# Optimization experiments

Measured on AMD Instinct MI355X. Metric: run time of the kernel, lower is better.

Reference implementation:

```python
import jax, jax.numpy as jnp
import numpy as np

B, S, HID = 16, 1, 2048
H, D = 32, 64
KV = 4096
SCALE = D ** -0.5


def setup_inputs() -> dict:
    key = jax.random.key(0)
    ks = jax.random.split(key, 5)
    x = jax.random.normal(ks[0], (B, S, HID), dtype=jnp.float32)
    bias = jax.random.normal(ks[1], (B, H, S, KV), dtype=jnp.float32)
    past_kv = jax.random.normal(ks[2], (2, B, H, KV, D), dtype=jnp.float32)
    # fused QKV projection weight: [3*H*D, hidden], no bias
    w_qkv = jax.random.normal(ks[3], (3 * H * D, HID), dtype=jnp.float32) * (HID ** -0.5)
    # output projection: [hidden, H*D]
    w_o = jax.random.normal(ks[4], (HID, H * D), dtype=jnp.float32) * (HID ** -0.5)
    return {"x": x, "bias": bias, "past_kv": past_kv, "w_qkv": w_qkv, "w_o": w_o}


def reference(x, bias, past_kv, w_qkv, w_o):
    # fused QKV projection: [B, S, 3*H*D]
    qkv = jnp.einsum('bsh,oh->bso', x, w_qkv)
    # -> [3, B, H, S, D]  (proj, heads interleaved as (proj heads head_dim))
    qkv = qkv.reshape(B, S, 3, H, D).transpose(2, 0, 3, 1, 4)
    q, k_new, v_new = qkv[0], qkv[1], qkv[2]
    # KV cache: keep first KV-1 entries, append current step's k/v as the last slot
    past_k = past_kv[0, :, :, : KV - 1]  # [B, H, KV-1, D]
    past_v = past_kv[1, :, :, : KV - 1]
    k = jnp.concatenate([past_k, k_new], axis=-2)  # [B, H, KV, D]
    v = jnp.concatenate([past_v, v_new], axis=-2)
    # SDPA with additive relative-position bias
    scores = jnp.einsum('bhqd,bhkd->bhqk', q, k) * SCALE + bias
    probs = jax.nn.softmax(scores, axis=-1)
    a = jnp.einsum('bhqk,bhkd->bhqd', probs, v)  # [B, H, S, D]
    a = a.transpose(0, 2, 1, 3).reshape(B, S, H * D)
    return jnp.einsum('bsf,of->bso', a, w_o)
```

## Files before the change

kernel.cpp:

```cpp
#include <hip/hip_runtime.h>
#include <math.h>

#define Bc     16
#define HIDc   2048
#define Hc     32
#define Dc     64
#define KVc    4096
#define QKVO   6144
#define SCALEc 0.125f
#define CHUNKS 4
#define CHUNK  1024

typedef float f4v __attribute__((ext_vector_type(4)));

__global__ __launch_bounds__(256) void qkv_kernel(const float* __restrict__ x,
                                                  const float* __restrict__ w,
                                                  float* __restrict__ qkv) {
    __shared__ float4 xs[512];
    int blk = blockIdx.x;
    int b   = blk & 15;
    int og  = blk >> 4;
    int t = threadIdx.x, lane = t & 63, wid = t >> 6;
    const float4* xr = reinterpret_cast<const float4*>(x + (size_t)b * HIDc);
    xs[t]       = xr[t];
    xs[t + 256] = xr[t + 256];
    __syncthreads();
    int o0 = og * 64 + wid * 16;
#pragma unroll 2
    for (int i = 0; i < 16; ++i) {
        int o = o0 + i;
        const float4* wr = reinterpret_cast<const float4*>(w + (size_t)o * HIDc);
        float acc = 0.f;
#pragma unroll
        for (int j = 0; j < 8; ++j) {
            float4 a = xs[lane + 64 * j];
            float4 c = wr[lane + 64 * j];
            acc += a.x * c.x + a.y * c.y + a.z * c.z + a.w * c.w;
        }
#pragma unroll
        for (int off = 32; off >= 1; off >>= 1) acc += __shfl_xor(acc, off);
        if (lane == 0) qkv[(size_t)b * QKVO + o] = acc;
    }
}

__global__ __launch_bounds__(256, 4) void attn_chunk_kernel(const float* __restrict__ qkv,
                                                            const float* __restrict__ bias,
                                                            const float* __restrict__ past_kv,
                                                            float* __restrict__ part_o,
                                                            float* __restrict__ part_s) {
    __shared__ float bs[CHUNK];
    __shared__ float accs[16][65];
    __shared__ float ps[16];

    int blk = blockIdx.x;
    int c   = blk & (CHUNKS - 1);
    int bh  = blk >> 2;
    int h   = bh & 31;
    int b   = bh >> 5;
    int t    = threadIdx.x;
    int lane = t & 63;
    int wid  = t >> 6;
    int sg   = lane >> 4;
    int cg   = lane & 15;
    int row0 = c * CHUNK;

    reinterpret_cast<float4*>(bs)[t] =
        reinterpret_cast<const float4*>(bias + (size_t)bh * KVc + row0)[t];

    const float* qp = qkv + (size_t)b * QKVO + h * Dc;
    float4 q4 = reinterpret_cast<const float4*>(qp)[cg];

    const size_t kvstride = (size_t)KVc * Dc;
    const float* pastK = past_kv + (size_t)bh * kvstride + (size_t)row0 * Dc;
    const float* pastV = past_kv + (size_t)(Bc * Hc) * kvstride + (size_t)bh * kvstride
                         + (size_t)row0 * Dc;

    __syncthreads();

    int rbase = wid * 4 + sg;
    float s = 0.f;
    float4 acc = {0.f, 0.f, 0.f, 0.f};

    f4v kA[4], vA[4], kB[4], vB[4];

    auto LOAD = [&](int ot, f4v (&k4)[4], f4v (&v4)[4]) {
        int it = ot * 4;
#pragma unroll
        for (int u = 0; u < 4; ++u) {
            int rl = (it + u) * 16 + rbase;
            k4[u] = __builtin_nontemporal_load(
                        reinterpret_cast<const f4v*>(pastK + (size_t)rl * Dc) + cg);
        }
#pragma unroll
        for (int u = 0; u < 4; ++u) {
            int rl = (it + u) * 16 + rbase;
            v4[u] = __builtin_nontemporal_load(
                        reinterpret_cast<const f4v*>(pastV + (size_t)rl * Dc) + cg);
        }
    };
    auto COMPUTE = [&](int ot, f4v (&k4)[4], f4v (&v4)[4]) {
        int it = ot * 4;
        float es = 0.f;
        float4 va = {0.f, 0.f, 0.f, 0.f};
#pragma unroll
        for (int u = 0; u < 4; ++u) {
            int rl = (it + u) * 16 + rbase;
            float pp = q4.x * k4[u].x + q4.y * k4[u].y + q4.z * k4[u].z + q4.w * k4[u].w;
            pp += __shfl_xor(pp, 1);
            pp += __shfl_xor(pp, 2);
            pp += __shfl_xor(pp, 4);
            pp += __shfl_xor(pp, 8);
            float e = __expf(fmaf(pp, SCALEc, bs[rl]));
            es += e;
            va.x = fmaf(e, v4[u].x, va.x);
            va.y = fmaf(e, v4[u].y, va.y);
            va.z = fmaf(e, v4[u].z, va.z);
            va.w = fmaf(e, v4[u].w, va.w);
        }
        s += es;
        acc.x += va.x;
        acc.y += va.y;
        acc.z += va.z;
        acc.w += va.w;
    };

    int nclean = (c == CHUNKS - 1) ? 15 : 16;
    LOAD(0, kA, vA);
    int ot = 0;
    while (true) {
        if (ot + 1 < nclean) LOAD(ot + 1, kB, vB);
        COMPUTE(ot, kA, vA);
        if (++ot >= nclean) break;
        if (ot + 1 < nclean) LOAD(ot + 1, kA, vA);
        COMPUTE(ot, kB, vB);
        if (++ot >= nclean) break;
    }

    if (c == CHUNKS - 1) {
        const float* knew = qkv + (size_t)b * QKVO + HIDc + h * Dc;
        const float* vnew = qkv + (size_t)b * QKVO + 2 * HIDc + h * Dc;
        int it = 60;
        float4 k4[4], v4[4];
#pragma unroll
        for (int u = 0; u < 4; ++u) {
            int rl = (it + u) * 16 + rbase;
            const float* kr = (rl == CHUNK - 1) ? knew : (pastK + (size_t)rl * Dc);
            k4[u] = reinterpret_cast<const float4*>(kr)[cg];
        }
#pragma unroll
        for (int u = 0; u < 4; ++u) {
            int rl = (it + u) * 16 + rbase;
            const float* vr = (rl == CHUNK - 1) ? vnew : (pastV + (size_t)rl * Dc);
            v4[u] = reinterpret_cast<const float4*>(vr)[cg];
        }
#pragma unroll
        for (int u = 0; u < 4; ++u) {
            int rl = (it + u) * 16 + rbase;
            float pp = q4.x * k4[u].x + q4.y * k4[u].y + q4.z * k4[u].z + q4.w * k4[u].w;
            pp += __shfl_xor(pp, 1);
            pp += __shfl_xor(pp, 2);
            pp += __shfl_xor(pp, 4);
            pp += __shfl_xor(pp, 8);
            float e = __expf(fmaf(pp, SCALEc, bs[rl]));
            s += e;
            acc.x = fmaf(e, v4[u].x, acc.x);
            acc.y = fmaf(e, v4[u].y, acc.y);
            acc.z = fmaf(e, v4[u].z, acc.z);
            acc.w = fmaf(e, v4[u].w, acc.w);
        }
    }

    int sgid = wid * 4 + sg;
    if (cg == 0) ps[sgid] = s;
    accs[sgid][cg * 4 + 0] = acc.x;
    accs[sgid][cg * 4 + 1] = acc.y;
    accs[sgid][cg * 4 + 2] = acc.z;
    accs[sgid][cg * 4 + 3] = acc.w;
    __syncthreads();
    if (t < 64) {
        float S = 0.f, o = 0.f;
#pragma unroll
        for (int i = 0; i < 16; ++i) {
            S += ps[i];
            o += accs[i][t];
        }
        part_o[((size_t)bh * CHUNKS + c) * Dc + t] = o;
        if (t == 0) part_s[(size_t)bh * CHUNKS + c] = S;
    }
}

__global__ __launch_bounds__(64) void attn_combine_kernel(const float* __restrict__ part_o,
                                                          const float* __restrict__ part_s,
                                                          float* __restrict__ attn_out) {
    int bh = blockIdx.x;
    int d  = threadIdx.x;
    float S = 0.f, o = 0.f;
#pragma unroll
    for (int c = 0; c < CHUNKS; ++c) {
        S += part_s[(size_t)bh * CHUNKS + c];
        o += part_o[((size_t)bh * CHUNKS + c) * Dc + d];
    }
    attn_out[(size_t)bh * Dc + d] = o / S;
}

__global__ __launch_bounds__(256) void outproj_kernel(const float* __restrict__ attn,
                                                      const float* __restrict__ w_o,
                                                      float* __restrict__ out) {
    __shared__ float4 as[512];
    int blk = blockIdx.x;
    int b   = blk & 15;
    int fg  = blk >> 4;
    int t = threadIdx.x, lane = t & 63, wid = t >> 6;
    const float4* ar = reinterpret_cast<const float4*>(attn + (size_t)b * HIDc);
    as[t]       = ar[t];
    as[t + 256] = ar[t + 256];
    __syncthreads();
    int f0 = fg * 64 + wid * 16;
#pragma unroll 2
    for (int i = 0; i < 16; ++i) {
        int f = f0 + i;
        const float4* wr = reinterpret_cast<const float4*>(w_o + (size_t)f * HIDc);
        float acc = 0.f;
#pragma unroll
        for (int j = 0; j < 8; ++j) {
            float4 a = as[lane + 64 * j];
            float4 c = wr[lane + 64 * j];
            acc += a.x * c.x + a.y * c.y + a.z * c.z + a.w * c.w;
        }
#pragma unroll
        for (int off = 32; off >= 1; off >>= 1) acc += __shfl_xor(acc, off);
        if (lane == 0) out[(size_t)b * HIDc + f] = acc;
    }
}

extern "C" void kernel_launch(void* const* d_in, const int* in_sizes, int n_in,
                              void* d_out, int out_size, void* d_ws, size_t ws_size,
                              hipStream_t stream) {
    const float* x       = (const float*)d_in[0];
    const float* bias    = (const float*)d_in[1];
    const float* past_kv = (const float*)d_in[2];
    const float* w_qkv   = (const float*)d_in[3];
    const float* w_o     = (const float*)d_in[4];
    float* out = (float*)d_out;

    float* qkv    = (float*)d_ws;
    float* attn   = qkv + (size_t)Bc * QKVO;
    float* part_o = attn + (size_t)Bc * HIDc;
    float* part_s = part_o + (size_t)Bc * Hc * CHUNKS * Dc;

    qkv_kernel<<<dim3(Bc * (QKVO / 64)), dim3(256), 0, stream>>>(x, w_qkv, qkv);
    attn_chunk_kernel<<<dim3(Bc * Hc * CHUNKS), dim3(256), 0, stream>>>(qkv, bias, past_kv, part_o, part_s);
    attn_combine_kernel<<<dim3(Bc * Hc), dim3(64), 0, stream>>>(part_o, part_s, attn);
    outproj_kernel<<<dim3(Bc * (HIDc / 64)), dim3(256), 0, stream>>>(attn, w_o, out);
}
```

Measured before the change: 245.5 us.

## Batch eight rows per block in GEMVs and fuse combine into out-projection

The QKV and output projection kernels now process eight batch rows per block, so each weight row is loaded once per eight batch rows instead of once per row. The split-KV combine step is folded into the output projection's shared-memory staging, removing a separate kernel launch and the intermediate attention buffer. The cost is a 64KB shared-memory footprint per block, fewer blocks, and more accumulator registers, which may reduce occupancy.

```diff
diff --git a/kernel.cpp b/kernel.cpp
--- a/kernel.cpp
+++ b/kernel.cpp
@@ -13,33 +13,42 @@
 
 typedef float f4v __attribute__((ext_vector_type(4)));
 
-__global__ __launch_bounds__(256) void qkv_kernel(const float* __restrict__ x,
-                                                  const float* __restrict__ w,
-                                                  float* __restrict__ qkv) {
-    __shared__ float4 xs[512];
+__global__ __launch_bounds__(256) void qkv_kernel2(const float* __restrict__ x,
+                                                   const float* __restrict__ w,
+                                                   float* __restrict__ qkv) {
+    __shared__ float4 xs[8 * 512];
     int blk = blockIdx.x;
-    int b   = blk & 15;
-    int og  = blk >> 4;
+    int bg  = blk & 1;
+    int rb  = blk >> 1;
     int t = threadIdx.x, lane = t & 63, wid = t >> 6;
-    const float4* xr = reinterpret_cast<const float4*>(x + (size_t)b * HIDc);
-    xs[t]       = xr[t];
-    xs[t + 256] = xr[t + 256];
-    __syncthreads();
-    int o0 = og * 64 + wid * 16;
+    const float4* xbase = reinterpret_cast<const float4*>(x) + (size_t)bg * 8 * 512;
+#pragma unroll
+    for (int i = 0; i < 16; ++i) xs[t + 256 * i] = xbase[t + 256 * i];
+    __syncthreads();
 #pragma unroll 2
-    for (int i = 0; i < 16; ++i) {
-        int o = o0 + i;
+    for (int rr = 0; rr < 4; ++rr) {
+        int o = rb * 16 + wid * 4 + rr;
         const float4* wr = reinterpret_cast<const float4*>(w + (size_t)o * HIDc);
-        float acc = 0.f;
+        float acc[8] = {0.f, 0.f, 0.f, 0.f, 0.f, 0.f, 0.f, 0.f};
 #pragma unroll
         for (int j = 0; j < 8; ++j) {
-            float4 a = xs[lane + 64 * j];
-            float4 c = wr[lane + 64 * j];
-            acc += a.x * c.x + a.y * c.y + a.z * c.z + a.w * c.w;
-        }
-#pragma unroll
-        for (int off = 32; off >= 1; off >>= 1) acc += __shfl_xor(acc, off);
-        if (lane == 0) qkv[(size_t)b * QKVO + o] = acc;
+            float4 wv = wr[lane + 64 * j];
+#pragma unroll
+            for (int bi = 0; bi < 8; ++bi) {
+                float4 xv = xs[bi * 512 + lane + 64 * j];
+                acc[bi] += wv.x * xv.x + wv.y * xv.y + wv.z * xv.z + wv.w * xv.w;
+            }
+        }
+#pragma unroll
+        for (int bi = 0; bi < 8; ++bi) {
+#pragma unroll
+            for (int off = 32; off >= 1; off >>= 1) acc[bi] += __shfl_xor(acc[bi], off);
+        }
+        if (lane == 0) {
+#pragma unroll
+            for (int bi = 0; bi < 8; ++bi)
+                qkv[(size_t)(bg * 8 + bi) * QKVO + o] = acc[bi];
+        }
     }
 }
 
@@ -189,47 +198,61 @@
     }
 }
 
-__global__ __launch_bounds__(64) void attn_combine_kernel(const float* __restrict__ part_o,
-                                                          const float* __restrict__ part_s,
-                                                          float* __restrict__ attn_out) {
-    int bh = blockIdx.x;
-    int d  = threadIdx.x;
-    float S = 0.f, o = 0.f;
-#pragma unroll
-    for (int c = 0; c < CHUNKS; ++c) {
-        S += part_s[(size_t)bh * CHUNKS + c];
-        o += part_o[((size_t)bh * CHUNKS + c) * Dc + d];
-    }
-    attn_out[(size_t)bh * Dc + d] = o / S;
-}
-
-__global__ __launch_bounds__(256) void outproj_kernel(const float* __restrict__ attn,
-                                                      const float* __restrict__ w_o,
-                                                      float* __restrict__ out) {
-    __shared__ float4 as[512];
+__global__ __launch_bounds__(256) void outproj_kernel2(const float* __restrict__ part_o,
+                                                       const float* __restrict__ part_s,
+                                                       const float* __restrict__ w_o,
+                                                       float* __restrict__ out) {
+    __shared__ float4 as[8 * 512];
     int blk = blockIdx.x;
-    int b   = blk & 15;
-    int fg  = blk >> 4;
+    int bg  = blk & 1;
+    int rb  = blk >> 1;
     int t = threadIdx.x, lane = t & 63, wid = t >> 6;
-    const float4* ar = reinterpret_cast<const float4*>(attn + (size_t)b * HIDc);
-    as[t]       = ar[t];
-    as[t + 256] = ar[t + 256];
-    __syncthreads();
-    int f0 = fg * 64 + wid * 16;
+
+#pragma unroll
+    for (int i = 0; i < 16; ++i) {
+        int idx = t + 256 * i;
+        int bi  = idx >> 9;
+        int c4  = idx & 511;
+        int h   = c4 >> 4;
+        int q4i = c4 & 15;
+        int bh  = (bg * 8 + bi) * Hc + h;
+        const float4* po = reinterpret_cast<const float4*>(part_o) + (size_t)bh * 64 + q4i;
+        float4 v0 = po[0], v1 = po[16], v2 = po[32], v3 = po[48];
+        float S = part_s[bh * 4 + 0] + part_s[bh * 4 + 1]
+                + part_s[bh * 4 + 2] + part_s[bh * 4 + 3];
+        float si = 1.0f / S;
+        float4 r;
+        r.x = (v0.x + v1.x + v2.x + v3.x) * si;
+        r.y = (v0.y + v1.y + v2.y + v3.y) * si;
+        r.z = (v0.z + v1.z + v2.z + v3.z) * si;
+        r.w = (v0.w + v1.w + v2.w + v3.w) * si;
+        as[idx] = r;
+    }
+    __syncthreads();
 #pragma unroll 2
-    for (int i = 0; i < 16; ++i) {
-        int f = f0 + i;
+    for (int rr = 0; rr < 4; ++rr) {
+        int f = rb * 16 + wid * 4 + rr;
         const float4* wr = reinterpret_cast<const float4*>(w_o + (size_t)f * HIDc);
-        float acc = 0.f;
+        float acc[8] = {0.f, 0.f, 0.f, 0.f, 0.f, 0.f, 0.f, 0.f};
 #pragma unroll
         for (int j = 0; j < 8; ++j) {
-            float4 a = as[lane + 64 * j];
-            float4 c = wr[lane + 64 * j];
-            acc += a.x * c.x + a.y * c.y + a.z * c.z + a.w * c.w;
-        }
-#pragma unroll
-        for (int off = 32; off >= 1; off >>= 1) acc += __shfl_xor(acc, off);
-        if (lane == 0) out[(size_t)b * HIDc + f] = acc;
+            float4 wv = wr[lane + 64 * j];
+#pragma unroll
+            for (int bi = 0; bi < 8; ++bi) {
+                float4 av = as[bi * 512 + lane + 64 * j];
+                acc[bi] += wv.x * av.x + wv.y * av.y + wv.z * av.z + wv.w * av.w;
+            }
+        }
+#pragma unroll
+        for (int bi = 0; bi < 8; ++bi) {
+#pragma unroll
+            for (int off = 32; off >= 1; off >>= 1) acc[bi] += __shfl_xor(acc[bi], off);
+        }
+        if (lane == 0) {
+#pragma unroll
+            for (int bi = 0; bi < 8; ++bi)
+                out[(size_t)(bg * 8 + bi) * HIDc + f] = acc[bi];
+        }
     }
 }
 
@@ -244,12 +267,10 @@
     float* out = (float*)d_out;
 
     float* qkv    = (float*)d_ws;
-    float* attn   = qkv + (size_t)Bc * QKVO;
-    float* part_o = attn + (size_t)Bc * HIDc;
+    float* part_o = qkv + (size_t)Bc * QKVO;
     float* part_s = part_o + (size_t)Bc * Hc * CHUNKS * Dc;
 
-    qkv_kernel<<<dim3(Bc * (QKVO / 64)), dim3(256), 0, stream>>>(x, w_qkv, qkv);
+    qkv_kernel2<<<dim3(768), dim3(256), 0, stream>>>(x, w_qkv, qkv);
     attn_chunk_kernel<<<dim3(Bc * Hc * CHUNKS), dim3(256), 0, stream>>>(qkv, bias, past_kv, part_o, part_s);
-    attn_combine_kernel<<<dim3(Bc * Hc), dim3(64), 0, stream>>>(part_o, part_s, attn);
-    outproj_kernel<<<dim3(Bc * (HIDc / 64)), dim3(256), 0, stream>>>(attn, w_o, out);
-}
+    outproj_kernel2<<<dim3(256), dim3(256), 0, stream>>>(part_o, part_s, w_o, out);
+}
```

After: 226.9 us. 1.08x faster.
